# Performance work log

Hardware: AMD Instinct MI355X
Metric: run time of the kernel (lower is better)

Reference implementation:

```python
import jax, jax.numpy as jnp
import numpy as np

NP, LP, ROUTINGS = 8, 16, 3
PAD = 2  # (kernel_size - 1) // 2 for kernel_size=5, stride=1


def _squash_2(t):
    # norm over LP axis (axis=3); torch: norm/(1+norm^2+1e-4) * t
    norm = jnp.linalg.norm(t, axis=3, keepdims=True)
    return norm / (1.0 + norm * norm + 1e-4) * t


def setup_inputs() -> dict:
    key = jax.random.key(0)
    k1, k2 = jax.random.split(key)
    x = jax.random.normal(k1, (4, 4, 16, 256, 256), dtype=jnp.float32)
    # conv weights initialized uniform [0, 0.1] as in the torch module
    W = jax.random.uniform(k2, (NP * LP, 16, 5, 5), dtype=jnp.float32) * 0.1
    return {"x": x, "W": W}


def reference(x, W):
    B, NC, LC, H, Wd = x.shape
    xf = x.reshape(B * NC, LC, H, Wd)
    votes = jax.lax.conv_general_dilated(
        xf, W, window_strides=(1, 1), padding=((PAD, PAD), (PAD, PAD)),
        dimension_numbers=("NCHW", "OIHW", "NCHW"))  # (B*NC, NP*LP, H, W)
    votes = votes.reshape(B, NC, NP, LP, H, Wd)
    sims = jnp.zeros((B, NC, NP, 1, H, Wd), dtype=x.dtype)
    parent = None
    for _ in range(ROUTINGS):
        c_ij = jax.nn.softmax(sims + 1e-4, axis=2)          # softmax over NP
        parent_bs = jnp.sum(c_ij * votes, axis=1, keepdims=True)  # sum over NC
        parent = _squash_2(parent_bs)                        # (B,1,NP,LP,H,W)
        sims = sims + jnp.sum(votes * parent, axis=3, keepdims=True)
    return parent[:, 0]  # squeeze NC axis -> (B, NP, LP, H, W)
```

## Files before the change

### kernel.cpp

```cpp
#include <hip/hip_runtime.h>

#define NPAR 8
#define LPAR 16
#define OCH 128
#define HH 256
#define WW 256
#define HWSZ (HH*WW)

typedef _Float16 f16x8 __attribute__((ext_vector_type(8)));
typedef _Float16 f16x4 __attribute__((ext_vector_type(4)));
typedef _Float16 f16x2 __attribute__((ext_vector_type(2)));
typedef float    f32x4 __attribute__((ext_vector_type(4)));

#define WBUF_HALVES 8192
#define XS_BASE 16384
#define SMEM_MAIN 24576
#define VROW 132
#define SMEM_HALVES_FUSED 16896

#if defined(__has_builtin)
#if __has_builtin(__builtin_amdgcn_fdot2)
#define HAVE_FDOT2 1
#endif
#if __has_builtin(__builtin_amdgcn_global_load_lds)
#define HAVE_GLL 1
#endif
#endif

__device__ __forceinline__ float fdot2_acc(f16x2 a, f16x2 b, float c) {
#ifdef HAVE_FDOT2
    return __builtin_amdgcn_fdot2(a, b, c, false);
#else
    return c + (float)a[0] * (float)b[0] + (float)a[1] * (float)b[1];
#endif
}

__device__ __forceinline__ f16x2 quad_sum4_pk(f16x2 v) {
    int t = __builtin_amdgcn_update_dpp(0, __builtin_bit_cast(int, v),
                                        0xB1, 0xF, 0xF, true);
    v = v + __builtin_bit_cast(f16x2, t);
    t = __builtin_amdgcn_update_dpp(0, __builtin_bit_cast(int, v),
                                    0x4E, 0xF, 0xF, true);
    v = v + __builtin_bit_cast(f16x2, t);
    return v;
}

__device__ __forceinline__ void stage16(const _Float16* gp, _Float16* lp, int lane) {
#ifdef HAVE_GLL
    __builtin_amdgcn_global_load_lds((const __attribute__((address_space(1))) void*)gp,
                                     (__attribute__((address_space(3))) void*)lp, 16, 0, 0);
#else
    *(f16x8*)(lp + lane * 8) = *(const f16x8*)gp;
#endif
}

__global__ void reorder_W_swz(const float* __restrict__ Wg,
                              _Float16* __restrict__ ws) {
    int idx = blockIdx.x * 256 + threadIdx.x;
    if (idx >= 13 * 128 * 32) return;
    const int j  = idx & 7;
    const int gI = (idx >> 3) & 3;
    const int oc = (idx >> 5) & 127;
    const int kk = idx >> 12;
    const int q  = ((gI ^ ((oc >> 2) & 3)) << 3) | j;
    const int tap = 2 * kk + (q >> 4);
    const int ci  = ((q >> 3) & 1) * 8 + (q & 7);
    const float v = (tap < 25) ? Wg[oc * 400 + ci * 25 + tap] : 0.f;
    ws[idx] = (_Float16)v;
}

__global__ void reorder_W_lin(const float* __restrict__ Wg,
                              _Float16* __restrict__ ws) {
    int idx = blockIdx.x * 256 + threadIdx.x;
    if (idx >= 13 * 128 * 32) return;
    const int q  = idx & 31;
    const int oc = (idx >> 5) & 127;
    const int kk = idx >> 12;
    const int tap = 2 * kk + (q >> 4);
    const int ci  = ((q >> 3) & 1) * 8 + (q & 7);
    const float v = (tap < 25) ? Wg[oc * 400 + ci * 25 + tap] : 0.f;
    ws[idx] = (_Float16)v;
}

__global__ __launch_bounds__(256)
void transpose_x_kernel(const float* __restrict__ x, _Float16* __restrict__ xh) {
    __shared__ _Float16 ts[4096];
    const int tid = threadIdx.x;
    const int bx  = blockIdx.x;
    const int b   = bx >> 10;
    const int h   = (bx >> 2) & 255;
    const int wt  = bx & 3;
    const int w0  = wt * 64;
    {
        const int wl = tid & 63, cq = tid >> 6;
        const float* src = x + (((size_t)(b * 64 + cq * 16) * 256 + h) * 256 + w0 + wl);
#pragma unroll
        for (int k = 0; k < 2; ++k) {
            f16x8 pk;
#pragma unroll
            for (int j = 0; j < 8; ++j)
                pk[j] = (_Float16)src[(size_t)(k * 8 + j) * HWSZ];
            const int gL = (cq * 2 + k) ^ (wl & 7);
            *(f16x8*)&ts[wl * 64 + gL * 8] = pk;
        }
    }
    __syncthreads();
    {
        const int wo = tid >> 2, gq = tid & 3;
        _Float16* dst = xh + (((size_t)(b * 260) + h + 2) * 260 + (w0 + wo + 2)) * 64 + gq * 16;
#pragma unroll
        for (int k = 0; k < 2; ++k) {
            const int gL = (gq * 2 + k) ^ (wo & 7);
            *(f16x8*)&dst[k * 8] = *(const f16x8*)&ts[wo * 64 + gL * 8];
        }
    }
}

__global__ __launch_bounds__(256, 3)
void capsule_mfma8_kernel(const _Float16* __restrict__ xh,
                          const _Float16* __restrict__ wsW,
                          float* __restrict__ out) {
    __shared__ _Float16 sm[SMEM_MAIN];

    const int tid = threadIdx.x;
    const int w   = tid >> 6;
    const int l   = tid & 63;

    const int blk   = ((blockIdx.x & 7) << 10) + (blockIdx.x >> 3);
    const int b     = blk >> 11;
    const int rt    = blk & 2047;
    const int hrow0 = (rt >> 4) << 1;
    const int w0    = (rt & 15) << 4;

    {
        const size_t bbase = ((size_t)(b * 260 + hrow0) * 260 + w0) * 64;
#pragma unroll
        for (int jj = 0; jj < 4; ++jj) {
            const int cidx = w * 4 + jj;
            if (cidx < 15) {
                const int G = cidx * 64 + l;
                const unsigned dyr = (unsigned)G / 160u;
                const unsigned rem = (unsigned)G - dyr * 160u;
                const int wp = rem >> 3, g = rem & 7;
                const int gsrc = g ^ (wp & 7);
                const _Float16* gp = xh + bbase + dyr * 16640u + wp * 64 + gsrc * 8;
                stage16(gp, &sm[XS_BASE + cidx * 512], l);
            }
        }
    }
    {
#pragma unroll
        for (int jj = 0; jj < 4; ++jj) {
            const int cidx = w * 4 + jj;
            const int G = cidx * 64 + l;
            stage16(wsW + G * 8, &sm[cidx * 512], l);
        }
    }
    __syncthreads();

    const int rwc = w >> 1;
    const int oh  = w & 1;
    const int kq  = l >> 4;
    const int ml  = l & 15;
    const bool hiT = (kq & 2) != 0;
    const int pxA = ml >> 2;
    const int colA = (ml & 3) * 16 + (kq & 1) * 8;
    const int swz  = (ml >> 2) & 3;
    const int wbL  = oh * 2048 + ml * 32 + ((kq ^ swz) << 3);

    f32x4 acc[4][4];
#pragma unroll
    for (int a = 0; a < 4; ++a)
#pragma unroll
        for (int bb = 0; bb < 4; ++bb)
            acc[a][bb] = (f32x4){0.f, 0.f, 0.f, 0.f};

#pragma unroll
    for (int ph = 0; ph < 7; ++ph) {
        if (ph < 6) {
            const int nxt = ph + 1;
            const int cpw = (nxt < 6) ? 4 : 2;
            const int dbase = ((nxt & 1) ? WBUF_HALVES : 0);
#pragma unroll
            for (int jj = 0; jj < 4; ++jj) {
                if (jj < cpw) {
                    const int cidx = w * cpw + jj;
                    const int G = cidx * 64 + l;
                    stage16(wsW + nxt * 8192 + G * 8, &sm[dbase + cidx * 512], l);
                }
            }
        }
        __builtin_amdgcn_s_setprio(1);
        const int nkk = (ph < 6) ? 2 : 1;
#pragma unroll
        for (int kkl = 0; kkl < nkk; ++kkl) {
            const int kk = 2 * ph + kkl;
            f16x8 bf[4];
            const int wb = ((ph & 1) ? WBUF_HALVES : 0) + kkl * 4096 + wbL;
#pragma unroll
            for (int bb = 0; bb < 4; ++bb)
                bf[bb] = *(const f16x8*)&sm[wb + bb * 512];

            const int t0 = 2 * kk;
            const int t1 = (2 * kk + 1 > 24) ? 24 : 2 * kk + 1;
            const int dy = hiT ? (t1 / 5) : (t0 / 5);
            const int dx = hiT ? (t1 % 5) : (t0 % 5);

            f16x8 af[4];
#pragma unroll
            for (int a = 0; a < 4; ++a) {
                const int wp = a * 4 + pxA + dx;
                af[a] = *(const f16x8*)&sm[XS_BASE + ((rwc + dy) * 20 + wp) * 64
                                           + (colA ^ ((wp & 7) << 3))];
            }
#pragma unroll
            for (int a = 0; a < 4; ++a)
#pragma unroll
                for (int bb = 0; bb < 4; ++bb)
                    acc[a][bb] = __builtin_amdgcn_mfma_f32_16x16x32_f16(
                        af[a], bf[bb], acc[a][bb], 0, 0, 0);
        }
        __builtin_amdgcn_s_setprio(0);
        __syncthreads();
    }

#pragma unroll
    for (int a = 0; a < 4; ++a) {
#pragma unroll
        for (int reg = 0; reg < 4; ++reg) {
            f16x4 pk;
#pragma unroll
            for (int bb = 0; bb < 4; ++bb) pk[bb] = (_Float16)acc[a][bb][reg];
            const int R = rwc * 64 + a * 16 + kq * 4 + reg;
            *(f16x4*)&sm[R * VROW + ml * 8 + oh * 4] = pk;
        }
    }
    __syncthreads();

    const int ncR = tid & 3;
    const int h   = (tid >> 2) & 1;
    const int pxx = (tid >> 3) & 15;
    const int rw  = tid >> 7;

    const int R = rw * 64 + pxx * 4 + ncR;
    f16x8 vh[8];
#pragma unroll
    for (int c8 = 0; c8 < 8; ++c8)
        vh[c8] = *(const f16x8*)&sm[R * VROW + (h * 8 + c8) * 8];

    float* outb = out + (size_t)b * OCH * HWSZ
                + (size_t)(hrow0 + rw) * WW + (w0 + pxx);

    float sims[NPAR];
#pragma unroll
    for (int i = 0; i < NPAR; ++i) sims[i] = 0.f;

#pragma unroll
    for (int it = 0; it < 3; ++it) {
        float e[NPAR];
        float inv = 0.f;
        if (it > 0) {
            float mx = fmaxf(fmaxf(fmaxf(sims[0], sims[1]), fmaxf(sims[2], sims[3])),
                             fmaxf(fmaxf(sims[4], sims[5]), fmaxf(sims[6], sims[7])));
            float se = 0.f;
#pragma unroll
            for (int i = 0; i < NPAR; ++i) { e[i] = __expf(sims[i] - mx); se += e[i]; }
            inv = 1.f / se;
        }
#pragma unroll
        for (int np_ = 0; np_ < NPAR; ++np_) {
            const float cf = (it == 0) ? 0.125f : e[np_] * inv;
            const f16x2 cp = (f16x2){(_Float16)cf, (_Float16)cf};
            float n2 = 0.f, dot = 0.f;
            f16x2 keep0 = (f16x2){(_Float16)0.f, (_Float16)0.f};
            f16x2 keep1 = keep0;
#pragma unroll
            for (int k = 0; k < 4; ++k) {
                const f16x2 vv = (f16x2){vh[2 * k][np_], vh[2 * k + 1][np_]};
                const f16x2 t2 = quad_sum4_pk(cp * vv);
                n2 = fdot2_acc(t2, t2, n2);
                if (it < 2) dot = fdot2_acc(vv, t2, dot);
                if (it == 2 && (k >> 1) == (ncR & 1)) {
                    if (k & 1) keep1 = t2; else keep0 = t2;
                }
            }
            n2 += __shfl_xor(n2, 4);
            const float scale = sqrtf(n2) / (1.f + n2 + 1e-4f);
            if (it < 2) {
                dot += __shfl_xor(dot, 4);
                sims[np_] += scale * dot;
            }
            if (it == 2 && (ncR >> 1) == h) {
                outb[(size_t)(np_ * LPAR + ncR * 4 + 0) * HWSZ] = scale * (float)keep0[0];
                outb[(size_t)(np_ * LPAR + ncR * 4 + 1) * HWSZ] = scale * (float)keep0[1];
                outb[(size_t)(np_ * LPAR + ncR * 4 + 2) * HWSZ] = scale * (float)keep1[0];
                outb[(size_t)(np_ * LPAR + ncR * 4 + 3) * HWSZ] = scale * (float)keep1[1];
            }
        }
    }
}

__device__ __forceinline__ int xs_addr6(int dyr, int wp, int col) {
    return (dyr * 20 + wp) * 64 + (col ^ ((wp & 7) << 3));
}

__global__ __launch_bounds__(256, 3)
void capsule_mfma6_kernel(const float* __restrict__ x,
                          const _Float16* __restrict__ wsf,
                          float* __restrict__ out) {
    __shared__ _Float16 sm[SMEM_HALVES_FUSED];

    const int tid = threadIdx.x;
    const int w   = tid >> 6;
    const int l   = tid & 63;

    const int blk   = ((blockIdx.x & 7) << 10) + (blockIdx.x >> 3);
    const int b     = blk >> 11;
    const int rt    = blk & 2047;
    const int hrow0 = (rt >> 4) << 1;
    const int w0    = (rt & 15) << 4;

    for (int i = 0; i < 15; ++i) {
        const unsigned idx = i * 256 + tid;
        const unsigned q   = idx / 20u;
        const int wp  = idx - q * 20u;
        const int cip = q & 7;
        const int t2  = q >> 3;
        const int nc  = t2 & 3;
        const int dyr = t2 >> 2;
        const int hh  = hrow0 + dyr - 2;
        const int wg  = w0 + wp - 2;
        const bool ok = (hh >= 0) && (hh < HH) && (wg >= 0) && (wg < WW);
        const float* src = x + (((size_t)(b * 4 + nc) * 16 + cip * 2) * HH + hh) * (size_t)WW + wg;
        const float v0 = ok ? src[0] : 0.f;
        const float v1 = ok ? src[HWSZ] : 0.f;
        *(f16x2*)&sm[xs_addr6(dyr, wp, nc * 16 + cip * 2)] =
            (f16x2){(_Float16)v0, (_Float16)v1};
    }
    __syncthreads();

    const int rwc = w >> 1;
    const int oh  = w & 1;
    const int p   = l >> 4;
    const int ml  = l & 15;
    const bool hiT = (p & 2) != 0;
    const int ciA = (p & 1) * 8;
    const int pxA = ml >> 2;
    const int ncA = ml & 3;
    const int bfbase = (oh * 64 + ml) * 32 + p * 8;

    f32x4 acc[4][4];
#pragma unroll
    for (int a = 0; a < 4; ++a)
#pragma unroll
        for (int bb = 0; bb < 4; ++bb)
            acc[a][bb] = (f32x4){0.f, 0.f, 0.f, 0.f};

#pragma unroll
    for (int kk = 0; kk < 13; ++kk) {
        f16x8 bf[4];
#pragma unroll
        for (int bb = 0; bb < 4; ++bb)
            bf[bb] = *(const f16x8*)&wsf[kk * 4096 + bb * 512 + bfbase];

        const int t0 = 2 * kk;
        const int t1 = (2 * kk + 1 > 24) ? 24 : 2 * kk + 1;
        const int dy = hiT ? (t1 / 5) : (t0 / 5);
        const int dx = hiT ? (t1 % 5) : (t0 % 5);

        f16x8 af[4];
#pragma unroll
        for (int a = 0; a < 4; ++a)
            af[a] = *(const f16x8*)&sm[xs_addr6(rwc + dy, a * 4 + pxA + dx, ncA * 16 + ciA)];

#pragma unroll
        for (int a = 0; a < 4; ++a)
#pragma unroll
            for (int bb = 0; bb < 4; ++bb)
                acc[a][bb] = __builtin_amdgcn_mfma_f32_16x16x32_f16(
                    af[a], bf[bb], acc[a][bb], 0, 0, 0);
    }
    __syncthreads();

#pragma unroll
    for (int a = 0; a < 4; ++a) {
#pragma unroll
        for (int reg = 0; reg < 4; ++reg) {
            f16x4 pk;
#pragma unroll
            for (int bb = 0; bb < 4; ++bb) pk[bb] = (_Float16)acc[a][bb][reg];
            const int R = rwc * 64 + a * 16 + p * 4 + reg;
            *(f16x4*)&sm[R * VROW + ml * 8 + oh * 4] = pk;
        }
    }
    __syncthreads();

    const int ncR = tid & 3;
    const int h   = (tid >> 2) & 1;
    const int pxx = (tid >> 3) & 15;
    const int rw  = tid >> 7;

    const int R = rw * 64 + pxx * 4 + ncR;
    f16x8 vh[8];
#pragma unroll
    for (int c8 = 0; c8 < 8; ++c8)
        vh[c8] = *(const f16x8*)&sm[R * VROW + (h * 8 + c8) * 8];

    float* outb = out + (size_t)b * OCH * HWSZ
                + (size_t)(hrow0 + rw) * WW + (w0 + pxx);

    float sims[NPAR];
#pragma unroll
    for (int i = 0; i < NPAR; ++i) sims[i] = 0.f;

#pragma unroll
    for (int it = 0; it < 3; ++it) {
        float mx = fmaxf(fmaxf(fmaxf(sims[0], sims[1]), fmaxf(sims[2], sims[3])),
                         fmaxf(fmaxf(sims[4], sims[5]), fmaxf(sims[6], sims[7])));
        float e[NPAR];
        float se = 0.f;
#pragma unroll
        for (int i = 0; i < NPAR; ++i) { e[i] = __expf(sims[i] - mx); se += e[i]; }
        const float inv = 1.f / se;

#pragma unroll
        for (int np_ = 0; np_ < NPAR; ++np_) {
            const float cf = e[np_] * inv;
            const f16x2 cp = (f16x2){(_Float16)cf, (_Float16)cf};
            float n2 = 0.f, dot = 0.f;
            f16x2 keep0 = (f16x2){(_Float16)0.f, (_Float16)0.f};
            f16x2 keep1 = keep0;
#pragma unroll
            for (int k = 0; k < 4; ++k) {
                const f16x2 vv = (f16x2){vh[2 * k][np_], vh[2 * k + 1][np_]};
                const f16x2 t2 = quad_sum4_pk(cp * vv);
                n2  = fdot2_acc(t2, t2, n2);
                dot = fdot2_acc(vv, t2, dot);
                if (it == 2 && (k >> 1) == (ncR & 1)) {
                    if (k & 1) keep1 = t2; else keep0 = t2;
                }
            }
            n2  += __shfl_xor(n2, 4);
            dot += __shfl_xor(dot, 4);
            const float scale = sqrtf(n2) / (1.f + n2 + 1e-4f);
            sims[np_] += scale * dot;

            if (it == 2 && (ncR >> 1) == h) {
                outb[(size_t)(np_ * LPAR + ncR * 4 + 0) * HWSZ] = scale * (float)keep0[0];
                outb[(size_t)(np_ * LPAR + ncR * 4 + 1) * HWSZ] = scale * (float)keep0[1];
                outb[(size_t)(np_ * LPAR + ncR * 4 + 2) * HWSZ] = scale * (float)keep1[0];
                outb[(size_t)(np_ * LPAR + ncR * 4 + 3) * HWSZ] = scale * (float)keep1[1];
            }
        }
    }
}

extern "C" void kernel_launch(void* const* d_in, const int* in_sizes, int n_in,
                              void* d_out, int out_size, void* d_ws, size_t ws_size,
                              hipStream_t stream) {
    const float* x  = (const float*)d_in[0];
    const float* Wg = (const float*)d_in[1];
    float* out = (float*)d_out;
    _Float16* ws = (_Float16*)d_ws;
    (void)in_sizes; (void)n_in; (void)out_size;

    const size_t XH_BYTES = (size_t)4 * 260 * 260 * 64 * 2;
    const size_t NEED = 131072 + XH_BYTES;

    if (ws_size >= NEED) {
        _Float16* xh = ws + 65536;
        hipLaunchKernelGGL(reorder_W_swz, dim3(208), dim3(256), 0, stream, Wg, ws);
        hipMemsetAsync((void*)xh, 0, XH_BYTES, stream);
        hipLaunchKernelGGL(transpose_x_kernel, dim3(4096), dim3(256), 0, stream, x, xh);
        hipLaunchKernelGGL(capsule_mfma8_kernel, dim3(8192), dim3(256), 0, stream,
                           xh, ws, out);
    } else {
        hipLaunchKernelGGL(reorder_W_lin, dim3(208), dim3(256), 0, stream, Wg, ws);
        hipLaunchKernelGGL(capsule_mfma6_kernel, dim3(8192), dim3(256), 0, stream,
                           x, ws, out);
    }
}
```

Baseline: 219.7 us.

## Read conv weights directly from global memory instead of double-buffered LDS staging

The main MFMA kernel no longer stages weight tiles into shared memory with a double-buffered pipeline and per-phase barriers. Each wave now loads its B fragments straight from the linearly laid out fp16 weights in global memory (expected to hit in cache) across a single 13-step loop. LDS use drops to the input tile only, which may allow more resident blocks. It also removes the uniform-coefficient multiply in the first routing iteration and applies the 1/8 factor after the reductions instead. The cost is global/L2 load latency inside the MFMA loop, which is no longer hidden by prefetch.

```diff
diff --git a/kernel.cpp b/kernel.cpp
--- a/kernel.cpp
+++ b/kernel.cpp
@@ -12,9 +12,7 @@
 typedef _Float16 f16x2 __attribute__((ext_vector_type(2)));
 typedef float    f32x4 __attribute__((ext_vector_type(4)));
 
-#define WBUF_HALVES 8192
-#define XS_BASE 16384
-#define SMEM_MAIN 24576
+#define SMEM_MAIN 16896
 #define VROW 132
 #define SMEM_HALVES_FUSED 16896
 
@@ -52,21 +50,6 @@
 #else
     *(f16x8*)(lp + lane * 8) = *(const f16x8*)gp;
 #endif
-}
-
-__global__ void reorder_W_swz(const float* __restrict__ Wg,
-                              _Float16* __restrict__ ws) {
-    int idx = blockIdx.x * 256 + threadIdx.x;
-    if (idx >= 13 * 128 * 32) return;
-    const int j  = idx & 7;
-    const int gI = (idx >> 3) & 3;
-    const int oc = (idx >> 5) & 127;
-    const int kk = idx >> 12;
-    const int q  = ((gI ^ ((oc >> 2) & 3)) << 3) | j;
-    const int tap = 2 * kk + (q >> 4);
-    const int ci  = ((q >> 3) & 1) * 8 + (q & 7);
-    const float v = (tap < 25) ? Wg[oc * 400 + ci * 25 + tap] : 0.f;
-    ws[idx] = (_Float16)v;
 }
 
 __global__ void reorder_W_lin(const float* __restrict__ Wg,
@@ -117,9 +100,9 @@
 }
 
 __global__ __launch_bounds__(256, 3)
-void capsule_mfma8_kernel(const _Float16* __restrict__ xh,
-                          const _Float16* __restrict__ wsW,
-                          float* __restrict__ out) {
+void capsule_mfma10_kernel(const _Float16* __restrict__ xh,
+                           const _Float16* __restrict__ wsW,
+                           float* __restrict__ out) {
     __shared__ _Float16 sm[SMEM_MAIN];
 
     const int tid = threadIdx.x;
@@ -144,16 +127,8 @@
                 const int wp = rem >> 3, g = rem & 7;
                 const int gsrc = g ^ (wp & 7);
                 const _Float16* gp = xh + bbase + dyr * 16640u + wp * 64 + gsrc * 8;
-                stage16(gp, &sm[XS_BASE + cidx * 512], l);
-            }
-        }
-    }
-    {
-#pragma unroll
-        for (int jj = 0; jj < 4; ++jj) {
-            const int cidx = w * 4 + jj;
-            const int G = cidx * 64 + l;
-            stage16(wsW + G * 8, &sm[cidx * 512], l);
+                stage16(gp, &sm[cidx * 512], l);
+            }
         }
     }
     __syncthreads();
@@ -165,8 +140,7 @@
     const bool hiT = (kq & 2) != 0;
     const int pxA = ml >> 2;
     const int colA = (ml & 3) * 16 + (kq & 1) * 8;
-    const int swz  = (ml >> 2) & 3;
-    const int wbL  = oh * 2048 + ml * 32 + ((kq ^ swz) << 3);
+    const int bfbase = (oh * 64 + ml) * 32 + kq * 8;
 
     f32x4 acc[4][4];
 #pragma unroll
@@ -176,53 +150,34 @@
             acc[a][bb] = (f32x4){0.f, 0.f, 0.f, 0.f};
 
 #pragma unroll
-    for (int ph = 0; ph < 7; ++ph) {
-        if (ph < 6) {
-            const int nxt = ph + 1;
-            const int cpw = (nxt < 6) ? 4 : 2;
-            const int dbase = ((nxt & 1) ? WBUF_HALVES : 0);
-#pragma unroll
-            for (int jj = 0; jj < 4; ++jj) {
-                if (jj < cpw) {
-                    const int cidx = w * cpw + jj;
-                    const int G = cidx * 64 + l;
-                    stage16(wsW + nxt * 8192 + G * 8, &sm[dbase + cidx * 512], l);
-                }
-            }
+    for (int kk = 0; kk < 13; ++kk) {
+        f16x8 bf[4];
+#pragma unroll
+        for (int bb = 0; bb < 4; ++bb)
+            bf[bb] = *(const f16x8*)&wsW[kk * 4096 + bb * 512 + bfbase];
+
+        const int t0 = 2 * kk;
+        const int t1 = (2 * kk + 1 > 24) ? 24 : 2 * kk + 1;
+        const int dy = hiT ? (t1 / 5) : (t0 / 5);
+        const int dx = hiT ? (t1 % 5) : (t0 % 5);
+
+        f16x8 af[4];
+#pragma unroll
+        for (int a = 0; a < 4; ++a) {
+            const int wp = a * 4 + pxA + dx;
+            af[a] = *(const f16x8*)&sm[((rwc + dy) * 20 + wp) * 64
+                                       + (colA ^ ((wp & 7) << 3))];
         }
         __builtin_amdgcn_s_setprio(1);
-        const int nkk = (ph < 6) ? 2 : 1;
-#pragma unroll
-        for (int kkl = 0; kkl < nkk; ++kkl) {
-            const int kk = 2 * ph + kkl;
-            f16x8 bf[4];
-            const int wb = ((ph & 1) ? WBUF_HALVES : 0) + kkl * 4096 + wbL;
+#pragma unroll
+        for (int a = 0; a < 4; ++a)
 #pragma unroll
             for (int bb = 0; bb < 4; ++bb)
-                bf[bb] = *(const f16x8*)&sm[wb + bb * 512];
-
-            const int t0 = 2 * kk;
-            const int t1 = (2 * kk + 1 > 24) ? 24 : 2 * kk + 1;
-            const int dy = hiT ? (t1 / 5) : (t0 / 5);
-            const int dx = hiT ? (t1 % 5) : (t0 % 5);
-
-            f16x8 af[4];
-#pragma unroll
-            for (int a = 0; a < 4; ++a) {
-                const int wp = a * 4 + pxA + dx;
-                af[a] = *(const f16x8*)&sm[XS_BASE + ((rwc + dy) * 20 + wp) * 64
-                                           + (colA ^ ((wp & 7) << 3))];
-            }
-#pragma unroll
-            for (int a = 0; a < 4; ++a)
-#pragma unroll
-                for (int bb = 0; bb < 4; ++bb)
-                    acc[a][bb] = __builtin_amdgcn_mfma_f32_16x16x32_f16(
-                        af[a], bf[bb], acc[a][bb], 0, 0, 0);
-        }
+                acc[a][bb] = __builtin_amdgcn_mfma_f32_16x16x32_f16(
+                    af[a], bf[bb], acc[a][bb], 0, 0, 0);
         __builtin_amdgcn_s_setprio(0);
-        __syncthreads();
-    }
+    }
+    __syncthreads();
 
 #pragma unroll
     for (int a = 0; a < 4; ++a) {
@@ -269,7 +224,7 @@
         }
 #pragma unroll
         for (int np_ = 0; np_ < NPAR; ++np_) {
-            const float cf = (it == 0) ? 0.125f : e[np_] * inv;
+            const float cf = (it == 0) ? 0.f : e[np_] * inv;
             const f16x2 cp = (f16x2){(_Float16)cf, (_Float16)cf};
             float n2 = 0.f, dot = 0.f;
             f16x2 keep0 = (f16x2){(_Float16)0.f, (_Float16)0.f};
@@ -277,7 +232,8 @@
 #pragma unroll
             for (int k = 0; k < 4; ++k) {
                 const f16x2 vv = (f16x2){vh[2 * k][np_], vh[2 * k + 1][np_]};
-                const f16x2 t2 = quad_sum4_pk(cp * vv);
+                const f16x2 sv = (it == 0) ? vv : (cp * vv);
+                const f16x2 t2 = quad_sum4_pk(sv);
                 n2 = fdot2_acc(t2, t2, n2);
                 if (it < 2) dot = fdot2_acc(vv, t2, dot);
                 if (it == 2 && (k >> 1) == (ncR & 1)) {
@@ -285,9 +241,11 @@
                 }
             }
             n2 += __shfl_xor(n2, 4);
+            if (it == 0) n2 *= 0.015625f;
             const float scale = sqrtf(n2) / (1.f + n2 + 1e-4f);
             if (it < 2) {
                 dot += __shfl_xor(dot, 4);
+                if (it == 0) dot *= 0.125f;
                 sims[np_] += scale * dot;
             }
             if (it == 2 && (ncR >> 1) == h) {
@@ -467,15 +425,15 @@
     const size_t XH_BYTES = (size_t)4 * 260 * 260 * 64 * 2;
     const size_t NEED = 131072 + XH_BYTES;
 
+    hipLaunchKernelGGL(reorder_W_lin, dim3(208), dim3(256), 0, stream, Wg, ws);
+
     if (ws_size >= NEED) {
         _Float16* xh = ws + 65536;
-        hipLaunchKernelGGL(reorder_W_swz, dim3(208), dim3(256), 0, stream, Wg, ws);
         hipMemsetAsync((void*)xh, 0, XH_BYTES, stream);
         hipLaunchKernelGGL(transpose_x_kernel, dim3(4096), dim3(256), 0, stream, x, xh);
-        hipLaunchKernelGGL(capsule_mfma8_kernel, dim3(8192), dim3(256), 0, stream,
+        hipLaunchKernelGGL(capsule_mfma10_kernel, dim3(8192), dim3(256), 0, stream,
                            xh, ws, out);
     } else {
-        hipLaunchKernelGGL(reorder_W_lin, dim3(208), dim3(256), 0, stream, Wg, ws);
         hipLaunchKernelGGL(capsule_mfma6_kernel, dim3(8192), dim3(256), 0, stream,
                            x, ws, out);
     }
```

After: 219.2 us (median of 2 runs). About the same (-0.2%).
